# Optimization experiments

Measured on AMD Instinct MI355X. Metric: run time of the kernel, lower is better.

The kernel has to match this reference:

```python
import jax, jax.numpy as jnp
import numpy as np
from functools import partial

STRIDES = (8, 16, 32)
SIZES = ((80, 80), (40, 40), (20, 20))
NUM_CLASSES = 80
NMS_THR = 0.65
SCORE_THR = 0.01
MAX_DET = 100  # fixed-size NMS output (padded; validity = scores > 0)


def setup_inputs() -> dict:
    key = jax.random.key(0)
    ks = jax.random.split(key, 9)
    B = 32
    out = {}
    for i, (h, w) in enumerate(SIZES):
        out[f"cls{i}"] = jax.random.normal(ks[3 * i], (B, NUM_CLASSES, h, w), jnp.float32)
        out[f"reg{i}"] = jax.random.normal(ks[3 * i + 1], (B, 4, h, w), jnp.float32)
        out[f"obj{i}"] = jax.random.normal(ks[3 * i + 2], (B, 1, h, w), jnp.float32)
    return out


def _grid_points():
    # MlvlPointGenerator.grid_priors(with_stride=True), offset=0: (x, y, stride, stride)
    pts = []
    for (h, w), s in zip(SIZES, STRIDES):
        xs = jnp.arange(w, dtype=jnp.float32) * s
        ys = jnp.arange(h, dtype=jnp.float32) * s
        xx, yy = jnp.meshgrid(xs, ys)  # [h, w], x varies fastest -> matches NHWC flatten
        st = jnp.full((h * w,), float(s), jnp.float32)
        pts.append(jnp.stack([xx.ravel(), yy.ravel(), st, st], axis=-1))
    return jnp.concatenate(pts, axis=0)  # [A, 4]


def _flatten(t, c):
    # [N, C, H, W] -> [N, H*W, C]  (permute(0,2,3,1).reshape)
    return t.transpose(0, 2, 3, 1).reshape(t.shape[0], -1, c)


def _decode(points, reg):
    # YOLOXBBoxDecoder: center = pred_xy * stride + point, wh = exp(pred_wh) * stride
    stride = points[:, 2:]                       # [A, 2]
    xys = reg[..., :2] * stride + points[:, :2]  # [B, A, 2]
    whs = jnp.exp(reg[..., 2:]) * stride         # [B, A, 2]
    return jnp.concatenate([xys - whs * 0.5, xys + whs * 0.5], axis=-1)  # x1y1x2y2


def _iou_one_vs_all(b, boxes):
    # b: [4], boxes: [A, 4]
    tl = jnp.maximum(b[:2], boxes[:, :2])
    br = jnp.minimum(b[2:], boxes[:, 2:])
    wh = jnp.clip(br - tl, 0.0)
    inter = wh[:, 0] * wh[:, 1]
    a1 = (b[2] - b[0]) * (b[3] - b[1])
    a2 = (boxes[:, 2] - boxes[:, 0]) * (boxes[:, 3] - boxes[:, 1])
    return inter / (a1 + a2 - inter + 1e-6)


def _nms_image(boxes, cls_scores, objectness):
    # boxes [A,4], cls_scores [A,C] (post-sigmoid), objectness [A] (post-sigmoid)
    max_scores = jnp.max(cls_scores, axis=1)
    labels = jnp.argmax(cls_scores, axis=1)
    scores = max_scores * objectness
    live = jnp.where(scores >= SCORE_THR, scores, -jnp.inf)  # score_thr filter

    # batched_nms: offset boxes per class so boxes of different labels never overlap
    offset = jax.lax.stop_gradient(jnp.max(jnp.abs(boxes)) + 1.0)
    boxes_off = jax.lax.stop_gradient(boxes) + labels.astype(boxes.dtype)[:, None] * offset

    def body(i, state):
        live, keep, kscores = state
        best = jnp.argmax(live)
        kscores = kscores.at[i].set(live[best])
        keep = keep.at[i].set(best)
        iou = _iou_one_vs_all(boxes_off[best], boxes_off)
        live = jnp.where(iou > NMS_THR, -jnp.inf, live)
        live = live.at[best].set(-jnp.inf)
        return live, keep, kscores

    keep0 = jnp.zeros((MAX_DET,), jnp.int32)
    ks0 = jnp.full((MAX_DET,), -jnp.inf, boxes.dtype)
    _, keep, kscores = jax.lax.fori_loop(0, MAX_DET, body, (live, keep0, ks0))

    valid = kscores > -jnp.inf
    out_boxes = jnp.where(valid[:, None], boxes[keep], 0.0)
    out_scores = jnp.where(valid, scores[keep], 0.0)
    out_labels = jnp.where(valid, labels[keep], -1)
    return out_boxes, out_scores, out_labels, valid


def _forward(cls0, cls1, cls2, reg0, reg1, reg2, obj0, obj1, obj2):
    B = cls0.shape[0]
    flat_cls = jax.nn.sigmoid(jnp.concatenate([_flatten(c, NUM_CLASSES) for c in (cls0, cls1, cls2)], axis=1))
    flat_reg = jnp.concatenate([_flatten(r, 4) for r in (reg0, reg1, reg2)], axis=1)
    flat_obj = jax.nn.sigmoid(jnp.concatenate([_flatten(o, 1) for o in (obj0, obj1, obj2)], axis=1))[..., 0]
    points = _grid_points()
    boxes = _decode(points, flat_reg)  # [B, A, 4]
    return jax.vmap(_nms_image)(boxes, flat_cls, flat_obj)


@jax.jit
def reference(cls0, cls1, cls2, reg0, reg1, reg2, obj0, obj1, obj2):
    return _forward(cls0, cls1, cls2, reg0, reg1, reg2, obj0, obj1, obj2)
```

## Files before the change

### kernel.cpp

```cpp
#include <hip/hip_runtime.h>
#include <cmath>

typedef unsigned int uint;
typedef unsigned long long ull;

#define BATCH 32
#define NA 8400
#define NC 80
#define MAXDET 100
#define NMSTHR 0.65f
#define SCTHR 0.01f
#define NEG_INF (-INFINITY)

#define NT 1024
#define NW (NT / 64)
#define EPT 9
#define NBINS 4096
#define CAP 512

__device__ __forceinline__ float stable_sigmoid(float x) {
    if (x >= 0.f) return 1.f / (1.f + expf(-x));
    float e = expf(x);
    return e / (1.f + e);
}

template<int HW, int W, int S>
__device__ __forceinline__ void decode4(
    const float* __restrict__ cls, const float* __restrict__ reg,
    const float* __restrict__ obj, int b, int p, int q, int ag,
    float4* __restrict__ wboxes, int* __restrict__ wlabels, uint* __restrict__ wkeys)
{
    const float* cbase = cls + (size_t)b * NC * HW + (size_t)(q * 20) * HW + p;
    float v[20];
    #pragma unroll
    for (int i = 0; i < 20; ++i) v[i] = cbase[(size_t)i * HW];
    float m = v[0]; int c = 0;
    #pragma unroll
    for (int i = 1; i < 20; ++i)
        if (v[i] > m) { m = v[i]; c = i; }
    c += q * 20;

    #pragma unroll
    for (int o = 1; o <= 2; o <<= 1) {
        float om = __shfl_xor(m, o);
        int   oc = __shfl_xor(c, o);
        if (om > m || (om == m && oc < c)) { m = om; c = oc; }
    }

    if (q == 0) {
        const float* rb = reg + (size_t)b * 4 * HW + p;
        float r0 = rb[0];
        float r1 = rb[HW];
        float r2 = rb[2 * (size_t)HW];
        float r3 = rb[3 * (size_t)HW];
        float ov = obj[(size_t)b * HW + p];

        int y = p / W;
        int x = p - y * W;
        float sc = stable_sigmoid(m) * stable_sigmoid(ov);
        float cx = r0 * (float)S + (float)x * (float)S;
        float cy = r1 * (float)S + (float)y * (float)S;
        float bw = expf(r2) * (float)S;
        float bh = expf(r3) * (float)S;

        wboxes[ag]  = make_float4(cx - bw * 0.5f, cy - bh * 0.5f,
                                  cx + bw * 0.5f, cy + bh * 0.5f);
        wlabels[ag] = c;
        wkeys[ag]   = (sc >= SCTHR) ? ~__float_as_uint(sc) : 0xFFFFFFFFu;
    }
}

__global__ __launch_bounds__(256) void decode_kernel(
    const float* __restrict__ cls0, const float* __restrict__ reg0, const float* __restrict__ obj0,
    const float* __restrict__ cls1, const float* __restrict__ reg1, const float* __restrict__ obj1,
    const float* __restrict__ cls2, const float* __restrict__ reg2, const float* __restrict__ obj2,
    float4* __restrict__ wboxes, int* __restrict__ wlabels, uint* __restrict__ wkeys)
{
    int gid = blockIdx.x * blockDim.x + threadIdx.x;
    int ag = gid >> 2;
    int q  = gid & 3;
    int b = ag / NA;
    int j = ag - b * NA;

    if (j < 6400)
        decode4<6400, 80, 8>(cls0, reg0, obj0, b, j, q, ag, wboxes, wlabels, wkeys);
    else if (j < 8000)
        decode4<1600, 40, 16>(cls1, reg1, obj1, b, j - 6400, q, ag, wboxes, wlabels, wkeys);
    else
        decode4<400, 20, 32>(cls2, reg2, obj2, b, j - 8000, q, ag, wboxes, wlabels, wkeys);
}

__global__ __launch_bounds__(NT) void nms_kernel(
    const float4* __restrict__ wboxes, const int* __restrict__ wlabels,
    const uint* __restrict__ wkeys, float* __restrict__ out)
{
    int b = blockIdx.x;
    int t = threadIdx.x;
    int lane = t & 63;
    int wv = t >> 6;
    const float4* boxes  = wboxes  + (size_t)b * NA;
    const int*    labels = wlabels + (size_t)b * NA;
    const uint*   keys   = wkeys   + (size_t)b * NA;

    __shared__ uint  s_hist[NBINS];
    __shared__ uint  s_cum[NBINS + 1];
    __shared__ uint  s_wsum[NW];
    __shared__ ull   s_skey[CAP];
    __shared__ float s_kbox[MAXDET][4];
    __shared__ float s_ka1[MAXDET];
    __shared__ int   s_kidx[MAXDET];
    __shared__ float s_kscr[MAXDET];
    __shared__ int   s_klab[MAXDET];
    __shared__ float s_red[NW];
    __shared__ float s_off;
    __shared__ int   s_kept, s_winlo, s_winhi, s_nsel;

    float m = 0.f;
    #pragma unroll
    for (int w = 0; w < EPT; ++w) {
        int e = t + w * NT;
        if (e < NA) {
            float4 v = boxes[e];
            m = fmaxf(m, fmaxf(fmaxf(fabsf(v.x), fabsf(v.y)),
                               fmaxf(fabsf(v.z), fabsf(v.w))));
        }
    }
    #pragma unroll
    for (int o = 32; o >= 1; o >>= 1) m = fmaxf(m, __shfl_xor(m, o));
    if (lane == 0) s_red[wv] = m;
    for (int i = t; i < NBINS; i += NT) s_hist[i] = 0;
    if (t == 0) { s_kept = 0; s_winlo = 0; }
    __syncthreads();
    if (t == 0) {
        float mm = 0.f;
        for (int w = 0; w < NW; ++w) mm = fmaxf(mm, s_red[w]);
        s_off = mm + 1.f;
    }
    #pragma unroll
    for (int w = 0; w < EPT; ++w) {
        int e = t + w * NT;
        if (e < NA) {
            uint k = keys[e];
            if (k != 0xFFFFFFFFu) atomicAdd(&s_hist[k >> 20], 1u);
        }
    }
    __syncthreads();
    float off = s_off;

    uint l0 = s_hist[4 * t], l1 = s_hist[4 * t + 1],
         l2 = s_hist[4 * t + 2], l3 = s_hist[4 * t + 3];
    uint L = l0 + l1 + l2 + l3;
    uint ls = L;
    #pragma unroll
    for (int o = 1; o < 64; o <<= 1) {
        uint v = __shfl_up(ls, o);
        if (lane >= o) ls += v;
    }
    if (lane == 63) s_wsum[wv] = ls;
    __syncthreads();
    if (t < NW) {
        uint v = s_wsum[t];
        uint vs = v;
        #pragma unroll
        for (int o = 1; o < NW; o <<= 1) {
            uint u = __shfl_up(vs, o);
            if ((t & 63) >= o) vs += u;
        }
        s_wsum[t] = vs - v;
    }
    __syncthreads();
    uint base = s_wsum[wv] + (ls - L);
    s_cum[4 * t]     = base;
    s_cum[4 * t + 1] = base + l0;
    s_cum[4 * t + 2] = base + l0 + l1;
    s_cum[4 * t + 3] = base + l0 + l1 + l2;
    if (t == NT - 1) s_cum[NBINS] = base + L;

    for (;;) {
        __syncthreads();
        int kept = s_kept, winlo = s_winlo;
        uint remaining = s_cum[NBINS] - s_cum[winlo];
        if (kept >= MAXDET || winlo >= NBINS || remaining == 0u) break;
        if (t == 0) { s_winhi = winlo + 1; s_nsel = 0; }
        if (t < CAP) s_skey[t] = ~0ull;
        __syncthreads();
        uint cl = s_cum[winlo];
        #pragma unroll
        for (int q = 0; q < 4; ++q) {
            int i = t + q * NT;
            if (i >= winlo && i < NBINS) {
                bool p0 = (s_cum[i + 1] - cl) <= (uint)CAP;
                bool p1 = (i + 1 < NBINS) && ((s_cum[i + 2] - cl) <= (uint)CAP);
                if (p0 && !p1) s_winhi = i + 1;
            }
        }
        __syncthreads();
        int winhi = s_winhi;

        #pragma unroll
        for (int w = 0; w < EPT; ++w) {
            int e = t + w * NT;
            bool q = false;
            uint k = 0;
            if (e < NA) {
                k = keys[e];
                if (k != 0xFFFFFFFFu) {
                    int bin = (int)(k >> 20);
                    q = (bin >= winlo && bin < winhi);
                }
            }
            ull mask = __ballot(q);
            if (mask) {
                int leader = __ffsll(mask) - 1;
                int pbase = 0;
                if (lane == leader) pbase = atomicAdd(&s_nsel, __popcll(mask));
                pbase = __shfl(pbase, leader);
                if (q) {
                    int pos = pbase + __popcll(mask & ((1ull << lane) - 1ull));
                    if (pos < CAP) s_skey[pos] = ((ull)k << 32) | (uint)e;
                }
            }
        }
        __syncthreads();
        int nsel = s_nsel; if (nsel > CAP) nsel = CAP;

        ull k = (t < CAP) ? s_skey[t] : ~0ull;
        for (int k2 = 2; k2 <= CAP; k2 <<= 1) {
            for (int j = k2 >> 1; j > 0; j >>= 1) {
                if (j >= 64) {
                    if (t < CAP) s_skey[t] = k;
                    __syncthreads();
                    if (t < CAP) {
                        ull kp = s_skey[t ^ j];
                        bool low = (t & j) == 0;
                        bool up  = (t & k2) == 0;
                        k = ((k < kp) == (low == up)) ? k : kp;
                    }
                    __syncthreads();
                } else if (t < CAP) {
                    ull kp = __shfl_xor(k, j);
                    bool low = (t & j) == 0;
                    bool up  = (t & k2) == 0;
                    k = ((k < kp) == (low == up)) ? k : kp;
                }
            }
        }
        if (t < CAP) s_skey[t] = k;
        __syncthreads();

        if (t < 64) {
            int kept2 = s_kept;
            for (int cb = 0; cb < nsel && kept2 < MAXDET; cb += 64) {
                int ci = cb + lane;
                ull sk = (ci < nsel) ? s_skey[ci] : ~0ull;
                bool has = (sk != ~0ull);
                int idx = 0, lab = 0;
                float sc = 0.f, c0 = 0.f, c1 = 0.f, c2 = 0.f, c3 = 0.f, ca = 0.f;
                if (has) {
                    idx = (int)(sk & 0xFFFFFFFFull);
                    sc  = __uint_as_float(~(uint)(sk >> 32));
                    float4 rb = boxes[idx];
                    lab = labels[idx];
                    float lo = (float)lab * off;
                    c0 = rb.x + lo; c1 = rb.y + lo; c2 = rb.z + lo; c3 = rb.w + lo;
                    ca = (c2 - c0) * (c3 - c1);
                    for (int q = 0; q < kept2; ++q) {
                        float tlx = fmaxf(s_kbox[q][0], c0);
                        float tly = fmaxf(s_kbox[q][1], c1);
                        float brx = fminf(s_kbox[q][2], c2);
                        float bry = fminf(s_kbox[q][3], c3);
                        float ww = fmaxf(brx - tlx, 0.f);
                        float hh = fmaxf(bry - tly, 0.f);
                        float inter = ww * hh;
                        float iou = inter / (s_ka1[q] + ca - inter + 1e-6f);
                        if (iou > NMSTHR) { has = false; break; }
                    }
                }
                ull am = __ballot(has);
                while (am && kept2 < MAXDET) {
                    int f = __ffsll(am) - 1;
                    float f0 = __shfl(c0, f), f1 = __shfl(c1, f);
                    float f2 = __shfl(c2, f), f3 = __shfl(c3, f);
                    float fa = __shfl(ca, f);
                    int   fidx = __shfl(idx, f);
                    int   flab = __shfl(lab, f);
                    float fsc  = __shfl(sc, f);
                    if (lane == 0) {
                        s_kbox[kept2][0] = f0; s_kbox[kept2][1] = f1;
                        s_kbox[kept2][2] = f2; s_kbox[kept2][3] = f3;
                        s_ka1[kept2] = fa; s_kidx[kept2] = fidx;
                        s_kscr[kept2] = fsc; s_klab[kept2] = flab;
                    }
                    kept2++;
                    if (lane == f) has = false;
                    if (has) {
                        float tlx = fmaxf(f0, c0), tly = fmaxf(f1, c1);
                        float brx = fminf(f2, c2), bry = fminf(f3, c3);
                        float ww = fmaxf(brx - tlx, 0.f), hh = fmaxf(bry - tly, 0.f);
                        float inter = ww * hh;
                        float iou = inter / (fa + ca - inter + 1e-6f);
                        if (iou > NMSTHR) has = false;
                    }
                    am = __ballot(has);
                }
            }
            if (lane == 0) s_kept = kept2;
        }
        __syncthreads();
        if (t == 0) s_winlo = s_winhi;
    }
    __syncthreads();

    if (t < MAXDET) {
        int kept = s_kept;
        float4 obx = make_float4(0.f, 0.f, 0.f, 0.f);
        float osc = 0.f, olab = -1.f, oval = 0.f;
        if (t < kept) {
            int idx = s_kidx[t];
            obx  = boxes[idx];
            osc  = s_kscr[t];
            olab = (float)s_klab[t];
            oval = 1.f;
        }
        float* ob = out + ((size_t)b * MAXDET + t) * 4;
        ob[0] = obx.x; ob[1] = obx.y; ob[2] = obx.z; ob[3] = obx.w;
        out[BATCH * MAXDET * 4 + b * MAXDET + t] = osc;
        out[BATCH * MAXDET * 5 + b * MAXDET + t] = olab;
        out[BATCH * MAXDET * 6 + b * MAXDET + t] = oval;
    }
}

extern "C" void kernel_launch(void* const* d_in, const int* in_sizes, int n_in,
                              void* d_out, int out_size, void* d_ws, size_t ws_size,
                              hipStream_t stream) {
    const float* cls0 = (const float*)d_in[0];
    const float* reg0 = (const float*)d_in[1];
    const float* obj0 = (const float*)d_in[2];
    const float* cls1 = (const float*)d_in[3];
    const float* reg1 = (const float*)d_in[4];
    const float* obj1 = (const float*)d_in[5];
    const float* cls2 = (const float*)d_in[6];
    const float* reg2 = (const float*)d_in[7];
    const float* obj2 = (const float*)d_in[8];

    char* ws = (char*)d_ws;
    size_t nBA = (size_t)BATCH * NA;
    float4* wboxes  = (float4*)ws;
    int*    wlabels = (int*)(ws + nBA * 16);
    uint*   wkeys   = (uint*)(ws + nBA * 20);

    int total = BATCH * NA * 4;
    decode_kernel<<<total / 256, 256, 0, stream>>>(
        cls0, reg0, obj0, cls1, reg1, obj1, cls2, reg2, obj2,
        wboxes, wlabels, wkeys);

    nms_kernel<<<BATCH, NT, 0, stream>>>(wboxes, wlabels, wkeys, (float*)d_out);
}
```

Before: 173.6 us.

## Vectorize decode, move histogram and box max into decode, precompute candidate boxes

The decode kernel now has each thread group handle four anchors with float4 loads. It also builds the per-image score histogram and the coordinate maximum using global atomics, which removes two full passes over the data from the single-block-per-image NMS kernel. The NMS block shrinks to 512 threads, and a parallel pass stores the offset candidate boxes and areas in shared memory so the serial single-wave suppression loop no longer does scattered global loads. In exchange there are global atomic contention, an extra memset, and fewer threads for the per-image selection passes.

```diff
diff --git a/kernel.cpp b/kernel.cpp
--- a/kernel.cpp
+++ b/kernel.cpp
@@ -6,15 +6,15 @@
 
 #define BATCH 32
 #define NA 8400
+#define QPI 2100
 #define NC 80
 #define MAXDET 100
 #define NMSTHR 0.65f
 #define SCTHR 0.01f
-#define NEG_INF (-INFINITY)
-
-#define NT 1024
+
+#define NT 512
 #define NW (NT / 64)
-#define EPT 9
+#define EPT 17
 #define NBINS 4096
 #define CAP 512
 
@@ -25,48 +25,90 @@
 }
 
 template<int HW, int W, int S>
-__device__ __forceinline__ void decode4(
+__device__ __forceinline__ void decode4v(
     const float* __restrict__ cls, const float* __restrict__ reg,
-    const float* __restrict__ obj, int b, int p, int q, int ag,
-    float4* __restrict__ wboxes, int* __restrict__ wlabels, uint* __restrict__ wkeys)
+    const float* __restrict__ obj, int b, int p0, int q, int ag0,
+    float4* __restrict__ wboxes, int* __restrict__ wlabels,
+    uint* __restrict__ wkeys, uint* __restrict__ hist, uint* __restrict__ amax)
 {
-    const float* cbase = cls + (size_t)b * NC * HW + (size_t)(q * 20) * HW + p;
-    float v[20];
+    const float* cbase = cls + (size_t)b * NC * HW + (size_t)(q * 20) * HW + p0;
+    float m[4];
+    int   c[4];
+    {
+        float4 v = *(const float4*)cbase;
+        m[0] = v.x; m[1] = v.y; m[2] = v.z; m[3] = v.w;
+        c[0] = c[1] = c[2] = c[3] = q * 20;
+    }
     #pragma unroll
-    for (int i = 0; i < 20; ++i) v[i] = cbase[(size_t)i * HW];
-    float m = v[0]; int c = 0;
-    #pragma unroll
-    for (int i = 1; i < 20; ++i)
-        if (v[i] > m) { m = v[i]; c = i; }
-    c += q * 20;
-
+    for (int i = 1; i < 20; ++i) {
+        float4 v = *(const float4*)(cbase + (size_t)i * HW);
+        int cc = q * 20 + i;
+        if (v.x > m[0]) { m[0] = v.x; c[0] = cc; }
+        if (v.y > m[1]) { m[1] = v.y; c[1] = cc; }
+        if (v.z > m[2]) { m[2] = v.z; c[2] = cc; }
+        if (v.w > m[3]) { m[3] = v.w; c[3] = cc; }
+    }
     #pragma unroll
     for (int o = 1; o <= 2; o <<= 1) {
-        float om = __shfl_xor(m, o);
-        int   oc = __shfl_xor(c, o);
-        if (om > m || (om == m && oc < c)) { m = om; c = oc; }
-    }
-
+        #pragma unroll
+        for (int jj = 0; jj < 4; ++jj) {
+            float om = __shfl_xor(m[jj], o);
+            int   oc = __shfl_xor(c[jj], o);
+            if (om > m[jj] || (om == m[jj] && oc < c[jj])) { m[jj] = om; c[jj] = oc; }
+        }
+    }
+
+    float mm = 0.f;
     if (q == 0) {
-        const float* rb = reg + (size_t)b * 4 * HW + p;
-        float r0 = rb[0];
-        float r1 = rb[HW];
-        float r2 = rb[2 * (size_t)HW];
-        float r3 = rb[3 * (size_t)HW];
-        float ov = obj[(size_t)b * HW + p];
-
-        int y = p / W;
-        int x = p - y * W;
-        float sc = stable_sigmoid(m) * stable_sigmoid(ov);
-        float cx = r0 * (float)S + (float)x * (float)S;
-        float cy = r1 * (float)S + (float)y * (float)S;
-        float bw = expf(r2) * (float)S;
-        float bh = expf(r3) * (float)S;
-
-        wboxes[ag]  = make_float4(cx - bw * 0.5f, cy - bh * 0.5f,
-                                  cx + bw * 0.5f, cy + bh * 0.5f);
-        wlabels[ag] = c;
-        wkeys[ag]   = (sc >= SCTHR) ? ~__float_as_uint(sc) : 0xFFFFFFFFu;
+        const float* rb = reg + (size_t)b * 4 * HW + p0;
+        float4 r0 = *(const float4*)(rb);
+        float4 r1 = *(const float4*)(rb + HW);
+        float4 r2 = *(const float4*)(rb + 2 * (size_t)HW);
+        float4 r3 = *(const float4*)(rb + 3 * (size_t)HW);
+        float4 ov = *(const float4*)(obj + (size_t)b * HW + p0);
+
+        int y  = p0 / W;
+        int x0 = p0 - y * W;
+
+        float r0a[4] = { r0.x, r0.y, r0.z, r0.w };
+        float r1a[4] = { r1.x, r1.y, r1.z, r1.w };
+        float r2a[4] = { r2.x, r2.y, r2.z, r2.w };
+        float r3a[4] = { r3.x, r3.y, r3.z, r3.w };
+        float ova[4] = { ov.x, ov.y, ov.z, ov.w };
+
+        uint k4[4];
+        int  l4[4];
+        #pragma unroll
+        for (int jj = 0; jj < 4; ++jj) {
+            float sc = stable_sigmoid(m[jj]) * stable_sigmoid(ova[jj]);
+            float cx = r0a[jj] * (float)S + (float)(x0 + jj) * (float)S;
+            float cy = r1a[jj] * (float)S + (float)y * (float)S;
+            float bw = expf(r2a[jj]) * (float)S;
+            float bh = expf(r3a[jj]) * (float)S;
+            float x1 = cx - bw * 0.5f, y1 = cy - bh * 0.5f;
+            float x2 = cx + bw * 0.5f, y2 = cy + bh * 0.5f;
+            wboxes[ag0 + jj] = make_float4(x1, y1, x2, y2);
+            mm = fmaxf(mm, fmaxf(fmaxf(fabsf(x1), fabsf(y1)),
+                                 fmaxf(fabsf(x2), fabsf(y2))));
+            l4[jj] = c[jj];
+            k4[jj] = (sc >= SCTHR) ? ~__float_as_uint(sc) : 0xFFFFFFFFu;
+        }
+        *(int4*)(wlabels + ag0)  = make_int4(l4[0], l4[1], l4[2], l4[3]);
+        *(uint4*)(wkeys + ag0)   = make_uint4(k4[0], k4[1], k4[2], k4[3]);
+        #pragma unroll
+        for (int jj = 0; jj < 4; ++jj)
+            if (k4[jj] != 0xFFFFFFFFu)
+                atomicAdd(&hist[(size_t)b * NBINS + (k4[jj] >> 20)], 1u);
+    }
+
+    int b0 = __shfl(b, 0);
+    int b1 = __shfl(b, 63);
+    if (b0 == b1) {
+        #pragma unroll
+        for (int o = 32; o >= 1; o >>= 1) mm = fmaxf(mm, __shfl_xor(mm, o));
+        if ((threadIdx.x & 63) == 0) atomicMax(&amax[b], __float_as_uint(mm));
+    } else if (q == 0) {
+        atomicMax(&amax[b], __float_as_uint(mm));
     }
 }
 
@@ -74,25 +116,32 @@
     const float* __restrict__ cls0, const float* __restrict__ reg0, const float* __restrict__ obj0,
     const float* __restrict__ cls1, const float* __restrict__ reg1, const float* __restrict__ obj1,
     const float* __restrict__ cls2, const float* __restrict__ reg2, const float* __restrict__ obj2,
-    float4* __restrict__ wboxes, int* __restrict__ wlabels, uint* __restrict__ wkeys)
+    float4* __restrict__ wboxes, int* __restrict__ wlabels, uint* __restrict__ wkeys,
+    uint* __restrict__ hist, uint* __restrict__ amax)
 {
-    int gid = blockIdx.x * blockDim.x + threadIdx.x;
-    int ag = gid >> 2;
-    int q  = gid & 3;
-    int b = ag / NA;
-    int j = ag - b * NA;
-
-    if (j < 6400)
-        decode4<6400, 80, 8>(cls0, reg0, obj0, b, j, q, ag, wboxes, wlabels, wkeys);
-    else if (j < 8000)
-        decode4<1600, 40, 16>(cls1, reg1, obj1, b, j - 6400, q, ag, wboxes, wlabels, wkeys);
+    int gid  = blockIdx.x * blockDim.x + threadIdx.x;
+    int quad = gid >> 2;
+    int q    = gid & 3;
+    int b    = quad / QPI;
+    int jq   = quad - b * QPI;
+    int j0   = jq * 4;
+    int ag0  = b * NA + j0;
+
+    if (j0 < 6400)
+        decode4v<6400, 80, 8>(cls0, reg0, obj0, b, j0, q, ag0,
+                              wboxes, wlabels, wkeys, hist, amax);
+    else if (j0 < 8000)
+        decode4v<1600, 40, 16>(cls1, reg1, obj1, b, j0 - 6400, q, ag0,
+                               wboxes, wlabels, wkeys, hist, amax);
     else
-        decode4<400, 20, 32>(cls2, reg2, obj2, b, j - 8000, q, ag, wboxes, wlabels, wkeys);
+        decode4v<400, 20, 32>(cls2, reg2, obj2, b, j0 - 8000, q, ag0,
+                              wboxes, wlabels, wkeys, hist, amax);
 }
 
 __global__ __launch_bounds__(NT) void nms_kernel(
     const float4* __restrict__ wboxes, const int* __restrict__ wlabels,
-    const uint* __restrict__ wkeys, float* __restrict__ out)
+    const uint* __restrict__ wkeys, const uint* __restrict__ hist,
+    const uint* __restrict__ amax, float* __restrict__ out)
 {
     int b = blockIdx.x;
     int t = threadIdx.x;
@@ -101,55 +150,26 @@
     const float4* boxes  = wboxes  + (size_t)b * NA;
     const int*    labels = wlabels + (size_t)b * NA;
     const uint*   keys   = wkeys   + (size_t)b * NA;
-
-    __shared__ uint  s_hist[NBINS];
-    __shared__ uint  s_cum[NBINS + 1];
-    __shared__ uint  s_wsum[NW];
-    __shared__ ull   s_skey[CAP];
-    __shared__ float s_kbox[MAXDET][4];
-    __shared__ float s_ka1[MAXDET];
-    __shared__ int   s_kidx[MAXDET];
-    __shared__ float s_kscr[MAXDET];
-    __shared__ int   s_klab[MAXDET];
-    __shared__ float s_red[NW];
-    __shared__ float s_off;
-    __shared__ int   s_kept, s_winlo, s_winhi, s_nsel;
-
-    float m = 0.f;
+    const uint*   h      = hist    + (size_t)b * NBINS;
+
+    __shared__ uint   s_cum[NBINS + 1];
+    __shared__ uint   s_wsum[NW];
+    __shared__ ull    s_skey[CAP];
+    __shared__ float4 s_cbox[CAP];
+    __shared__ float  s_ca[CAP];
+    __shared__ int    s_clb[CAP];
+    __shared__ float  s_kbox[MAXDET][4];
+    __shared__ float  s_ka1[MAXDET];
+    __shared__ int    s_kidx[MAXDET];
+    __shared__ float  s_kscr[MAXDET];
+    __shared__ int    s_klab[MAXDET];
+    __shared__ float  s_off;
+    __shared__ int    s_kept, s_winlo, s_winhi, s_nsel;
+
+    uint l[8];
+    uint L = 0;
     #pragma unroll
-    for (int w = 0; w < EPT; ++w) {
-        int e = t + w * NT;
-        if (e < NA) {
-            float4 v = boxes[e];
-            m = fmaxf(m, fmaxf(fmaxf(fabsf(v.x), fabsf(v.y)),
-                               fmaxf(fabsf(v.z), fabsf(v.w))));
-        }
-    }
-    #pragma unroll
-    for (int o = 32; o >= 1; o >>= 1) m = fmaxf(m, __shfl_xor(m, o));
-    if (lane == 0) s_red[wv] = m;
-    for (int i = t; i < NBINS; i += NT) s_hist[i] = 0;
-    if (t == 0) { s_kept = 0; s_winlo = 0; }
-    __syncthreads();
-    if (t == 0) {
-        float mm = 0.f;
-        for (int w = 0; w < NW; ++w) mm = fmaxf(mm, s_red[w]);
-        s_off = mm + 1.f;
-    }
-    #pragma unroll
-    for (int w = 0; w < EPT; ++w) {
-        int e = t + w * NT;
-        if (e < NA) {
-            uint k = keys[e];
-            if (k != 0xFFFFFFFFu) atomicAdd(&s_hist[k >> 20], 1u);
-        }
-    }
-    __syncthreads();
-    float off = s_off;
-
-    uint l0 = s_hist[4 * t], l1 = s_hist[4 * t + 1],
-         l2 = s_hist[4 * t + 2], l3 = s_hist[4 * t + 3];
-    uint L = l0 + l1 + l2 + l3;
+    for (int i = 0; i < 8; ++i) { l[i] = h[8 * t + i]; L += l[i]; }
     uint ls = L;
     #pragma unroll
     for (int o = 1; o < 64; o <<= 1) {
@@ -157,6 +177,10 @@
         if (lane >= o) ls += v;
     }
     if (lane == 63) s_wsum[wv] = ls;
+    if (t == 0) {
+        s_kept = 0; s_winlo = 0;
+        s_off = __uint_as_float(amax[b]) + 1.f;
+    }
     __syncthreads();
     if (t < NW) {
         uint v = s_wsum[t];
@@ -164,17 +188,17 @@
         #pragma unroll
         for (int o = 1; o < NW; o <<= 1) {
             uint u = __shfl_up(vs, o);
-            if ((t & 63) >= o) vs += u;
+            if (t >= o) vs += u;
         }
         s_wsum[t] = vs - v;
     }
     __syncthreads();
-    uint base = s_wsum[wv] + (ls - L);
-    s_cum[4 * t]     = base;
-    s_cum[4 * t + 1] = base + l0;
-    s_cum[4 * t + 2] = base + l0 + l1;
-    s_cum[4 * t + 3] = base + l0 + l1 + l2;
-    if (t == NT - 1) s_cum[NBINS] = base + L;
+    {
+        uint run = s_wsum[wv] + (ls - L);
+        #pragma unroll
+        for (int i = 0; i < 8; ++i) { s_cum[8 * t + i] = run; run += l[i]; }
+        if (t == NT - 1) s_cum[NBINS] = run;
+    }
 
     for (;;) {
         __syncthreads();
@@ -182,12 +206,12 @@
         uint remaining = s_cum[NBINS] - s_cum[winlo];
         if (kept >= MAXDET || winlo >= NBINS || remaining == 0u) break;
         if (t == 0) { s_winhi = winlo + 1; s_nsel = 0; }
-        if (t < CAP) s_skey[t] = ~0ull;
+        s_skey[t] = ~0ull;
         __syncthreads();
         uint cl = s_cum[winlo];
         #pragma unroll
-        for (int q = 0; q < 4; ++q) {
-            int i = t + q * NT;
+        for (int qq = 0; qq < 8; ++qq) {
+            int i = t + qq * NT;
             if (i >= winlo && i < NBINS) {
                 bool p0 = (s_cum[i + 1] - cl) <= (uint)CAP;
                 bool p1 = (i + 1 < NBINS) && ((s_cum[i + 2] - cl) <= (uint)CAP);
@@ -200,22 +224,22 @@
         #pragma unroll
         for (int w = 0; w < EPT; ++w) {
             int e = t + w * NT;
-            bool q = false;
+            bool qf = false;
             uint k = 0;
             if (e < NA) {
                 k = keys[e];
                 if (k != 0xFFFFFFFFu) {
                     int bin = (int)(k >> 20);
-                    q = (bin >= winlo && bin < winhi);
+                    qf = (bin >= winlo && bin < winhi);
                 }
             }
-            ull mask = __ballot(q);
+            ull mask = __ballot(qf);
             if (mask) {
                 int leader = __ffsll(mask) - 1;
                 int pbase = 0;
                 if (lane == leader) pbase = atomicAdd(&s_nsel, __popcll(mask));
                 pbase = __shfl(pbase, leader);
-                if (q) {
+                if (qf) {
                     int pos = pbase + __popcll(mask & ((1ull << lane) - 1ull));
                     if (pos < CAP) s_skey[pos] = ((ull)k << 32) | (uint)e;
                 }
@@ -224,20 +248,18 @@
         __syncthreads();
         int nsel = s_nsel; if (nsel > CAP) nsel = CAP;
 
-        ull k = (t < CAP) ? s_skey[t] : ~0ull;
+        ull k = s_skey[t];
         for (int k2 = 2; k2 <= CAP; k2 <<= 1) {
             for (int j = k2 >> 1; j > 0; j >>= 1) {
                 if (j >= 64) {
-                    if (t < CAP) s_skey[t] = k;
+                    s_skey[t] = k;
                     __syncthreads();
-                    if (t < CAP) {
-                        ull kp = s_skey[t ^ j];
-                        bool low = (t & j) == 0;
-                        bool up  = (t & k2) == 0;
-                        k = ((k < kp) == (low == up)) ? k : kp;
-                    }
+                    ull kp = s_skey[t ^ j];
+                    bool low = (t & j) == 0;
+                    bool up  = (t & k2) == 0;
+                    k = ((k < kp) == (low == up)) ? k : kp;
                     __syncthreads();
-                } else if (t < CAP) {
+                } else {
                     ull kp = __shfl_xor(k, j);
                     bool low = (t & j) == 0;
                     bool up  = (t & k2) == 0;
@@ -245,7 +267,24 @@
                 }
             }
         }
-        if (t < CAP) s_skey[t] = k;
+        s_skey[t] = k;
+        __syncthreads();
+
+        float off = s_off;
+        if (t < nsel) {
+            ull sk = s_skey[t];
+            if (sk != ~0ull) {
+                int idx = (int)(sk & 0xFFFFFFFFull);
+                float4 rb = boxes[idx];
+                int lb = labels[idx];
+                float lo = (float)lb * off;
+                float c0 = rb.x + lo, c1 = rb.y + lo;
+                float c2 = rb.z + lo, c3 = rb.w + lo;
+                s_cbox[t] = make_float4(c0, c1, c2, c3);
+                s_ca[t]   = (c2 - c0) * (c3 - c1);
+                s_clb[t]  = lb;
+            }
+        }
         __syncthreads();
 
         if (t < 64) {
@@ -259,20 +298,19 @@
                 if (has) {
                     idx = (int)(sk & 0xFFFFFFFFull);
                     sc  = __uint_as_float(~(uint)(sk >> 32));
-                    float4 rb = boxes[idx];
-                    lab = labels[idx];
-                    float lo = (float)lab * off;
-                    c0 = rb.x + lo; c1 = rb.y + lo; c2 = rb.z + lo; c3 = rb.w + lo;
-                    ca = (c2 - c0) * (c3 - c1);
-                    for (int q = 0; q < kept2; ++q) {
-                        float tlx = fmaxf(s_kbox[q][0], c0);
-                        float tly = fmaxf(s_kbox[q][1], c1);
-                        float brx = fminf(s_kbox[q][2], c2);
-                        float bry = fminf(s_kbox[q][3], c3);
+                    float4 cbx = s_cbox[ci];
+                    c0 = cbx.x; c1 = cbx.y; c2 = cbx.z; c3 = cbx.w;
+                    ca = s_ca[ci];
+                    lab = s_clb[ci];
+                    for (int qq = 0; qq < kept2; ++qq) {
+                        float tlx = fmaxf(s_kbox[qq][0], c0);
+                        float tly = fmaxf(s_kbox[qq][1], c1);
+                        float brx = fminf(s_kbox[qq][2], c2);
+                        float bry = fminf(s_kbox[qq][3], c3);
                         float ww = fmaxf(brx - tlx, 0.f);
                         float hh = fmaxf(bry - tly, 0.f);
                         float inter = ww * hh;
-                        float iou = inter / (s_ka1[q] + ca - inter + 1e-6f);
+                        float iou = inter / (s_ka1[qq] + ca - inter + 1e-6f);
                         if (iou > NMSTHR) { has = false; break; }
                     }
                 }
@@ -348,11 +386,16 @@
     float4* wboxes  = (float4*)ws;
     int*    wlabels = (int*)(ws + nBA * 16);
     uint*   wkeys   = (uint*)(ws + nBA * 20);
-
-    int total = BATCH * NA * 4;
+    uint*   whist   = (uint*)(ws + nBA * 24);
+    uint*   wamax   = (uint*)(ws + nBA * 24 + (size_t)BATCH * NBINS * 4);
+
+    hipMemsetAsync(whist, 0, (size_t)BATCH * NBINS * 4 + 128, stream);
+
+    int total = BATCH * QPI * 4;
     decode_kernel<<<total / 256, 256, 0, stream>>>(
         cls0, reg0, obj0, cls1, reg1, obj1, cls2, reg2, obj2,
-        wboxes, wlabels, wkeys);
-
-    nms_kernel<<<BATCH, NT, 0, stream>>>(wboxes, wlabels, wkeys, (float*)d_out);
+        wboxes, wlabels, wkeys, whist, wamax);
+
+    nms_kernel<<<BATCH, NT, 0, stream>>>(wboxes, wlabels, wkeys, whist, wamax,
+                                         (float*)d_out);
 }
```

Result: slower. 221.2 us (+27.4%).
